# Optimization experiments

Hardware: AMD Instinct MI355X
Metric: run time of the kernel (lower is better)

## Reference

```python
import jax, jax.numpy as jnp
import numpy as np

D_STATE = 16
DT_RANK = 48
D_CONV = 4
EPS = 1e-5


def rmsnorm(x, w):
    return x * jax.lax.rsqrt(jnp.mean(x * x, axis=-1, keepdims=True) + EPS) * w


def causal_dw_conv(u, w, b):
    # u: [B,T,D], w: [D,K] depthwise causal kernel, b: [D]
    B, T, D = u.shape
    K = w.shape[1]
    up = jnp.pad(u, ((0, 0), (K - 1, 0), (0, 0)))
    acc = jnp.zeros_like(u)
    for k in range(K):  # K=4, tiny fixed loop
        acc = acc + up[:, k:k + T, :] * w[:, k]
    return acc + b


def mamba_mixer(h, ipw, cw, cb, xpw, dpw, dpb, alog, dpar, opw):
    # h: [B,T,d_model]
    B, T, _ = h.shape
    xz = h @ ipw.T                       # [B,T,2*d_inner]
    u, z = jnp.split(xz, 2, axis=-1)     # each [B,T,d_inner]
    u = jax.nn.silu(causal_dw_conv(u, cw, cb))
    xp = u @ xpw.T                       # [B,T,dt_rank+2*d_state]
    dt = xp[..., :DT_RANK]
    Bm = xp[..., DT_RANK:DT_RANK + D_STATE]
    Cm = xp[..., DT_RANK + D_STATE:]
    delta = jax.nn.softplus(dt @ dpw.T + dpb)      # [B,T,d_inner]
    A = -jnp.exp(alog)                              # [d_inner, d_state], negative
    dA = jnp.exp(delta[..., None] * A)              # [B,T,d_inner,d_state] in (0,1)
    dBu = (delta * u)[..., None] * Bm[:, :, None, :]
    # time-major for scan
    dA_t = jnp.moveaxis(dA, 1, 0)
    dBu_t = jnp.moveaxis(dBu, 1, 0)
    C_t = jnp.moveaxis(Cm, 1, 0)

    def step(hst, inp):
        a, bu, c = inp
        hst = a * hst + bu                          # [B,d_inner,d_state]
        y = jnp.einsum('bdn,bn->bd', hst, c)
        return hst, y

    h0 = jnp.zeros((B, u.shape[-1], D_STATE), u.dtype)
    _, ys = jax.lax.scan(step, h0, (dA_t, dBu_t, C_t))
    y = jnp.moveaxis(ys, 0, 1) + u * dpar           # skip via D
    y = y * jax.nn.silu(z)                          # gate
    return y @ opw.T                                # [B,T,d_model]


def setup_inputs() -> dict:
    key = jax.random.key(0)
    ks = jax.random.split(key, 16)
    L, d_model, d_inner = 4, 768, 1536
    B, C, T = 4, 256, 512
    s = 0.02
    return {
        'x': jax.random.normal(ks[0], (B, C, T), jnp.float32),
        'in_proj_w': jax.random.normal(ks[1], (L, 2 * d_inner, d_model), jnp.float32) * s,
        'conv_w': jax.random.normal(ks[2], (L, d_inner, D_CONV), jnp.float32) * 0.3,
        'conv_b': jnp.zeros((L, d_inner), jnp.float32),
        'x_proj_w': jax.random.normal(ks[3], (L, DT_RANK + 2 * D_STATE, d_inner), jnp.float32) * s,
        'dt_proj_w': jax.random.normal(ks[4], (L, d_inner, DT_RANK), jnp.float32) * 0.1,
        'dt_proj_b': jax.random.normal(ks[5], (L, d_inner), jnp.float32) * 0.1 - 4.0,
        'A_log': jax.random.uniform(ks[6], (L, d_inner, D_STATE), jnp.float32, 0.0, 1.5),
        'D_param': jax.random.uniform(ks[7], (L, d_inner), jnp.float32),
        'out_proj_w': jax.random.normal(ks[8], (L, d_model, d_inner), jnp.float32) * s,
        'norm_w': jnp.ones((L, d_model), jnp.float32),
        'norm_f_w': jnp.ones((d_model,), jnp.float32),
        'inp_w': jax.random.normal(ks[9], (d_model, C), jnp.float32) * s,
        'inp_b': jnp.zeros((d_model,), jnp.float32),
        'cls_w': jax.random.normal(ks[10], (10, d_model), jnp.float32) * s,
        'cls_b': jnp.zeros((10,), jnp.float32),
    }


def reference(x, in_proj_w, conv_w, conv_b, x_proj_w, dt_proj_w, dt_proj_b,
              A_log, D_param, out_proj_w, norm_w, norm_f_w,
              inp_w, inp_b, cls_w, cls_b):
    # x: (B, C, T) -> (B, T, C)
    xt = jnp.transpose(x, (0, 2, 1))
    h = xt @ inp_w.T + inp_b                # [B,T,d_model]
    hidden = h
    residual = None
    L = in_proj_w.shape[0]
    for l in range(L):
        residual = hidden if residual is None else hidden + residual
        normed = rmsnorm(residual, norm_w[l])
        hidden = mamba_mixer(normed, in_proj_w[l], conv_w[l], conv_b[l],
                             x_proj_w[l], dt_proj_w[l], dt_proj_b[l],
                             A_log[l], D_param[l], out_proj_w[l])
    residual = hidden + residual
    hidden = rmsnorm(residual, norm_f_w)
    pooled = hidden.mean(axis=1)            # [B,d_model]
    logits = pooled @ cls_w.T + cls_b       # [B,num_labels]
    return logits
```

## Files before the change

### kernel.cpp

```cpp
#include <hip/hip_runtime.h>
#include <math.h>

#define D_MODEL 768
#define D_INNER 1536
#define B_SZ 4
#define T_SZ 512
#define ROWS (B_SZ*T_SZ)
#define XP_N 80
#define CH 32
#define CT 16
#define XS 8
#define XKC (D_INNER/XS)
#define OS 4
#define OKC (D_INNER/OS)
#define MN_OUT (ROWS*768)

typedef __attribute__((ext_vector_type(8))) short bf16x8;
typedef __attribute__((ext_vector_type(4))) float f32x4;

#define GLL(g, l) __builtin_amdgcn_global_load_lds( \
    (const __attribute__((address_space(1))) void*)(g), \
    (__attribute__((address_space(3))) void*)(l), 16, 0, 0)

__device__ __forceinline__ float sigmoidf_(float x){ return 1.0f/(1.0f+__expf(-x)); }
__device__ __forceinline__ float siluf_(float x){ return x*sigmoidf_(x); }
__device__ __forceinline__ unsigned short f2bf(float f){
  unsigned u = __builtin_bit_cast(unsigned, f);
  u = (u + 0x7FFFu + ((u >> 16) & 1u)) >> 16;
  return (unsigned short)u;
}

__global__ __launch_bounds__(256) void gemm_bf16(
    const unsigned short* __restrict__ A, const unsigned short* __restrict__ Wb,
    float* __restrict__ C, int M, int N, int K)
{
  __shared__ unsigned short As[64*32];
  __shared__ unsigned short Ws[128*32];
  const int tid = threadIdx.x;
  const int bm = blockIdx.y*64, bn = blockIdx.x*128;
  const int wave = tid >> 6, lane = tid & 63;
  const int wn = wave*32;
  const int fr = lane & 15, quad = lane >> 4;
  f32x4 acc[4][2] = {};
  const int chunk = wave*64 + lane;
  const int row0 = chunk >> 2;
  const int khp  = chunk & 3;
  const int khl  = (khp + 4 - ((row0 >> 1) & 3)) & 3;
  const unsigned short* Ag = A  + (size_t)(bm + row0)*K + khl*8;
  const unsigned short* Wg = Wb + (size_t)(bn + row0)*K + khl*8;
  const size_t rstep = (size_t)64*K;
  unsigned short* ldsA = As + wave*512;
  unsigned short* ldsW = Ws + wave*512;

  for (int k0 = 0; k0 < K; k0 += 32){
    GLL(Ag + k0,          ldsA);
    GLL(Wg + k0,          ldsW);
    GLL(Wg + rstep + k0,  ldsW + 2048);
    __syncthreads();
    bf16x8 a[4], b[2];
    #pragma unroll
    for (int i=0;i<4;i++){
      const int row = i*16 + fr;
      a[i] = *(const bf16x8*)(As + row*32 + (((quad + (row>>1)) & 3)*8));
    }
    #pragma unroll
    for (int j=0;j<2;j++){
      const int row = wn + j*16 + fr;
      b[j] = *(const bf16x8*)(Ws + row*32 + (((quad + (row>>1)) & 3)*8));
    }
    #pragma unroll
    for (int i=0;i<4;i++)
      #pragma unroll
      for (int j=0;j<2;j++)
        acc[i][j] = __builtin_amdgcn_mfma_f32_16x16x32_bf16(a[i], b[j], acc[i][j], 0, 0, 0);
    __syncthreads();
  }
  #pragma unroll
  for (int i=0;i<4;i++){
    #pragma unroll
    for (int r=0;r<4;r++){
      const int row = bm + i*16 + quad*4 + r;
      float* Cp = C + (size_t)row*N + bn + wn + fr;
      #pragma unroll
      for (int j=0;j<2;j++)
        Cp[j*16] = acc[i][j][r];
    }
  }
}

__global__ __launch_bounds__(256) void gemm_bf16_sk(
    const unsigned short* __restrict__ A, const unsigned short* __restrict__ Wb,
    float* __restrict__ P0, float* __restrict__ P1, int M, int N, int K)
{
  __shared__ unsigned short As[64*32];
  __shared__ unsigned short Ws[128*32];
  const int tid = threadIdx.x;
  const int bm = blockIdx.y*64, bn = blockIdx.x*128;
  const int s = blockIdx.z;
  const int koff = s*OKC;
  const int wave = tid >> 6, lane = tid & 63;
  const int wn = wave*32;
  const int fr = lane & 15, quad = lane >> 4;
  f32x4 acc[4][2] = {};
  const int chunk = wave*64 + lane;
  const int row0 = chunk >> 2;
  const int khp  = chunk & 3;
  const int khl  = (khp + 4 - ((row0 >> 1) & 3)) & 3;
  const unsigned short* Ag = A  + (size_t)(bm + row0)*K + koff + khl*8;
  const unsigned short* Wg = Wb + (size_t)(bn + row0)*K + koff + khl*8;
  const size_t rstep = (size_t)64*K;
  unsigned short* ldsA = As + wave*512;
  unsigned short* ldsW = Ws + wave*512;

  for (int k0 = 0; k0 < OKC; k0 += 32){
    GLL(Ag + k0,          ldsA);
    GLL(Wg + k0,          ldsW);
    GLL(Wg + rstep + k0,  ldsW + 2048);
    __syncthreads();
    bf16x8 a[4], b[2];
    #pragma unroll
    for (int i=0;i<4;i++){
      const int row = i*16 + fr;
      a[i] = *(const bf16x8*)(As + row*32 + (((quad + (row>>1)) & 3)*8));
    }
    #pragma unroll
    for (int j=0;j<2;j++){
      const int row = wn + j*16 + fr;
      b[j] = *(const bf16x8*)(Ws + row*32 + (((quad + (row>>1)) & 3)*8));
    }
    #pragma unroll
    for (int i=0;i<4;i++)
      #pragma unroll
      for (int j=0;j<2;j++)
        acc[i][j] = __builtin_amdgcn_mfma_f32_16x16x32_bf16(a[i], b[j], acc[i][j], 0, 0, 0);
    __syncthreads();
  }
  float* Cb = (s < 2 ? P0 : P1) + (size_t)(s & 1)*MN_OUT;
  #pragma unroll
  for (int i=0;i<4;i++){
    #pragma unroll
    for (int r=0;r<4;r++){
      const int row = bm + i*16 + quad*4 + r;
      float* Cp = Cb + (size_t)row*N + bn + wn + fr;
      #pragma unroll
      for (int j=0;j<2;j++)
        Cp[j*16] = acc[i][j][r];
    }
  }
}

__global__ __launch_bounds__(256) void sgemm_input(
    const float* __restrict__ x, const float* __restrict__ W,
    const float* __restrict__ bias, float* __restrict__ C)
{
  __shared__ float As[16][64];
  __shared__ float Wsh[16][64];
  const int bm = blockIdx.y*64, bn = blockIdx.x*64;
  const int b = bm >> 9, t0 = bm & (T_SZ-1);
  const int tid = threadIdx.x;
  const int tx = tid & 15, ty = tid >> 4;
  const int lm = tid & 63, lk = (tid >> 6) << 2;
  float acc[4][4] = {};
  const float* Wp = W + (size_t)(bn+lm)*256 + lk;
  const float* xb = x + ((size_t)b*256)*512 + t0 + lm;
  for (int k0 = 0; k0 < 256; k0 += 16){
    #pragma unroll
    for (int i=0;i<4;i++)
      As[lk+i][lm] = xb[(size_t)(k0+lk+i)*512];
    float4 wv = *(const float4*)(Wp + k0);
    Wsh[lk+0][lm]=wv.x; Wsh[lk+1][lm]=wv.y; Wsh[lk+2][lm]=wv.z; Wsh[lk+3][lm]=wv.w;
    __syncthreads();
    #pragma unroll
    for (int k = 0; k < 16; k++){
      float a[4], w[4];
      #pragma unroll
      for (int i=0;i<4;i++) a[i] = As[k][ty*4+i];
      #pragma unroll
      for (int j=0;j<4;j++) w[j] = Wsh[k][tx*4+j];
      #pragma unroll
      for (int i=0;i<4;i++)
        #pragma unroll
        for (int j=0;j<4;j++)
          acc[i][j] += a[i]*w[j];
    }
    __syncthreads();
  }
  #pragma unroll
  for (int i=0;i<4;i++){
    const int r = bm + ty*4 + i;
    #pragma unroll
    for (int j=0;j<4;j++){
      const int n = bn + tx*4 + j;
      C[(size_t)r*768 + n] = acc[i][j] + bias[n];
    }
  }
}

__global__ __launch_bounds__(256) void xproj_conv_splitk(
    const float* __restrict__ xz, const float* __restrict__ cw,
    const float* __restrict__ cb, const float* __restrict__ W,
    float* __restrict__ part)
{
  __shared__ float As[16][64];
  __shared__ float Wsh[16][80];
  const int bm = blockIdx.x*64;
  const int s = blockIdx.y;
  const int koff = s*XKC;
  const int tid = threadIdx.x;
  const int tx = tid & 15, ty = tid >> 4;
  const int lm = tid & 63, lk = (tid >> 6) << 2;
  float acc[4][5] = {};
  const int row = bm + lm;
  const int t = row & (T_SZ-1);
  for (int k0 = 0; k0 < XKC; k0 += 16){
    const int d0 = koff + k0 + lk;
    float4 cbv = *(const float4*)(cb + d0);
    float cba[4] = {cbv.x, cbv.y, cbv.z, cbv.w};
    float4 tp3 = *(const float4*)(xz + (size_t)row*3072 + d0);
    float4 tp0 = (t>=3) ? *(const float4*)(xz + (size_t)(row-3)*3072 + d0) : make_float4(0.f,0.f,0.f,0.f);
    float4 tp1 = (t>=2) ? *(const float4*)(xz + (size_t)(row-2)*3072 + d0) : make_float4(0.f,0.f,0.f,0.f);
    float4 tp2 = (t>=1) ? *(const float4*)(xz + (size_t)(row-1)*3072 + d0) : make_float4(0.f,0.f,0.f,0.f);
    float a0[4]={tp0.x,tp0.y,tp0.z,tp0.w}, a1[4]={tp1.x,tp1.y,tp1.z,tp1.w};
    float a2[4]={tp2.x,tp2.y,tp2.z,tp2.w}, a3[4]={tp3.x,tp3.y,tp3.z,tp3.w};
    #pragma unroll
    for (int i=0;i<4;i++){
      const float4 w4 = *(const float4*)(cw + (size_t)(d0+i)*4);
      float a = cba[i];
      a += a0[i]*w4.x; a += a1[i]*w4.y; a += a2[i]*w4.z; a += a3[i]*w4.w;
      As[lk+i][lm] = siluf_(a);
    }
    for (int i = tid; i < 320; i += 256){
      const int wr = i % 80, wk = (i / 80) << 2;
      float4 wv = *(const float4*)(W + (size_t)wr*D_INNER + koff + k0 + wk);
      Wsh[wk+0][wr]=wv.x; Wsh[wk+1][wr]=wv.y; Wsh[wk+2][wr]=wv.z; Wsh[wk+3][wr]=wv.w;
    }
    __syncthreads();
    #pragma unroll
    for (int k = 0; k < 16; k++){
      float a[4], w[5];
      #pragma unroll
      for (int i=0;i<4;i++) a[i] = As[k][ty*4+i];
      #pragma unroll
      for (int j=0;j<5;j++) w[j] = Wsh[k][tx*5+j];
      #pragma unroll
      for (int i=0;i<4;i++)
        #pragma unroll
        for (int j=0;j<5;j++)
          acc[i][j] += a[i]*w[j];
    }
    __syncthreads();
  }
  #pragma unroll
  for (int i=0;i<4;i++){
    const int r = bm + ty*4 + i;
    #pragma unroll
    for (int j=0;j<5;j++){
      const int n = tx*5 + j;
      part[((size_t)s*ROWS + r)*XP_N + n] = acc[i][j];
    }
  }
}

__global__ __launch_bounds__(256) void dtproj_fused(
    const float* __restrict__ part, const float* __restrict__ W,
    const float* __restrict__ bias, float* __restrict__ delta,
    float* __restrict__ xpbc)
// ... 46 lines not shown
  #pragma unroll
  for (int i=0;i<4;i++){
    const int r = bm + ty*4 + i;
    #pragma unroll
    for (int j=0;j<4;j++){
      const int n = bn + tx*4 + j;
      float v = acc[i][j] + bias[n];
      v = (v > 20.f) ? v : log1pf(__expf(v));
      delta[(size_t)r*D_INNER + n] = v;
    }
  }
}

__global__ __launch_bounds__(256) void scan_pass1(
    const float* __restrict__ delta, const float* __restrict__ xz,
    const float* __restrict__ xpbc, const float* __restrict__ alog,
    const float* __restrict__ cw, const float* __restrict__ cb,
    float* __restrict__ Pend, float* __restrict__ Hend)
{
  const int d = blockIdx.x*256 + threadIdx.x;
  const int b = blockIdx.y, c = blockIdx.z;
  float4 t0 = *(const float4*)(alog + d*16 + 0);
  float4 t1 = *(const float4*)(alog + d*16 + 4);
  float4 t2 = *(const float4*)(alog + d*16 + 8);
  float4 t3 = *(const float4*)(alog + d*16 + 12);
  float Av[16] = {t0.x,t0.y,t0.z,t0.w,t1.x,t1.y,t1.z,t1.w,
                  t2.x,t2.y,t2.z,t2.w,t3.x,t3.y,t3.z,t3.w};
  float h[16];
  #pragma unroll
  for (int n=0;n<16;n++){ Av[n] = -__expf(Av[n]); h[n]=0.f; }
  float sdv = 0.f;
  const size_t row0 = (size_t)b*T_SZ + (size_t)c*CT;
  const float* dp  = delta + row0*D_INNER + d;
  const float* xp0 = xz    + row0*3072 + d;
  const float* bp  = xpbc  + row0*32;
  const float4 cwv = *(const float4*)(cw + (size_t)d*4);
  const float cbv = cb[d];
  float xm3, xm2, xm1;
  if (c == 0){ xm3 = xm2 = xm1 = 0.f; }
  else { xm3 = xp0[-3*3072]; xm2 = xp0[-2*3072]; xm1 = xp0[-1*3072]; }
  #pragma unroll 4
  for (int tt=0; tt<CT; tt++){
    const float dv = dp[(size_t)tt*D_INNER];
    const float xc = xp0[(size_t)tt*3072];
    float ua = cbv;
    ua += xm3*cwv.x; ua += xm2*cwv.y; ua += xm1*cwv.z; ua += xc*cwv.w;
    const float uv = siluf_(ua);
    xm3 = xm2; xm2 = xm1; xm1 = xc;
    const float4 B0 = *(const float4*)(bp + (size_t)tt*32);
    const float4 B1 = *(const float4*)(bp + (size_t)tt*32 + 4);
    const float4 B2 = *(const float4*)(bp + (size_t)tt*32 + 8);
    const float4 B3 = *(const float4*)(bp + (size_t)tt*32 + 12);
    const float Bv[16] = {B0.x,B0.y,B0.z,B0.w,B1.x,B1.y,B1.z,B1.w,
                          B2.x,B2.y,B2.z,B2.w,B3.x,B3.y,B3.z,B3.w};
    const float du = dv*uv;
    sdv += dv;
    #pragma unroll
    for (int n=0;n<16;n++){
      const float dA = __expf(dv*Av[n]);
      h[n] = dA*h[n] + du*Bv[n];
    }
  }
  float P[16];
  #pragma unroll
  for (int n=0;n<16;n++) P[n] = __expf(Av[n]*sdv);
  float* Pp = Pend + ((size_t)(b*CH+c)*D_INNER + d)*16;
  float* Hp = Hend + ((size_t)(b*CH+c)*D_INNER + d)*16;
  *(float4*)(Pp+ 0) = make_float4(P[0],P[1],P[2],P[3]);
  *(float4*)(Pp+ 4) = make_float4(P[4],P[5],P[6],P[7]);
  *(float4*)(Pp+ 8) = make_float4(P[8],P[9],P[10],P[11]);
  *(float4*)(Pp+12) = make_float4(P[12],P[13],P[14],P[15]);
  *(float4*)(Hp+ 0) = make_float4(h[0],h[1],h[2],h[3]);
  *(float4*)(Hp+ 4) = make_float4(h[4],h[5],h[6],h[7]);
  *(float4*)(Hp+ 8) = make_float4(h[8],h[9],h[10],h[11]);
  *(float4*)(Hp+12) = make_float4(h[12],h[13],h[14],h[15]);
}

__global__ __launch_bounds__(256) void scan_combine(
    const float* __restrict__ Pend, const float* __restrict__ Hend,
    float* __restrict__ Hin)
{
  const int gid = blockIdx.x*256 + threadIdx.x;
  const int b = gid / (D_INNER*16);
  const int r = gid % (D_INNER*16);
  const size_t base = (size_t)b*CH*D_INNER*16 + r;
  const size_t step = (size_t)D_INNER*16;
  float h = 0.f;
  Hin[base] = 0.f;
  #pragma unroll
  for (int c=0; c<CH-1; c++){
    h = Pend[base + (size_t)c*step]*h + Hend[base + (size_t)c*step];
    Hin[base + (size_t)(c+1)*step] = h;
  }
}

__global__ __launch_bounds__(256) void scan_pass3(
    const float* __restrict__ delta, const float* __restrict__ xz,
    const float* __restrict__ xpbc, const float* __restrict__ alog,
    const float* __restrict__ cw, const float* __restrict__ cb,
    const float* __restrict__ Dp, const float* __restrict__ Hin,
    unsigned short* __restrict__ yb)
{
  const int d = blockIdx.x*256 + threadIdx.x;
  const int b = blockIdx.y, c = blockIdx.z;
  float4 t0 = *(const float4*)(alog + d*16 + 0);
  float4 t1 = *(const float4*)(alog + d*16 + 4);
  float4 t2 = *(const float4*)(alog + d*16 + 8);
  float4 t3 = *(const float4*)(alog + d*16 + 12);
  float Av[16] = {t0.x,t0.y,t0.z,t0.w,t1.x,t1.y,t1.z,t1.w,
                  t2.x,t2.y,t2.z,t2.w,t3.x,t3.y,t3.z,t3.w};
  #pragma unroll
  for (int n=0;n<16;n++) Av[n] = -__expf(Av[n]);
  const float* Hp = Hin + ((size_t)(b*CH+c)*D_INNER + d)*16;
  float4 h0 = *(const float4*)(Hp+0);
  float4 h1 = *(const float4*)(Hp+4);
  float4 h2 = *(const float4*)(Hp+8);
  float4 h3 = *(const float4*)(Hp+12);
  float h[16] = {h0.x,h0.y,h0.z,h0.w,h1.x,h1.y,h1.z,h1.w,
                 h2.x,h2.y,h2.z,h2.w,h3.x,h3.y,h3.z,h3.w};
  const float Dv = Dp[d];
  const size_t row0 = (size_t)b*T_SZ + (size_t)c*CT;
  const float* dp  = delta + row0*D_INNER + d;
  const float* xp0 = xz    + row0*3072 + d;
  const float* zp  = xz    + row0*3072 + 1536 + d;
  const float* bp  = xpbc  + row0*32;
  unsigned short* yp = yb + row0*D_INNER + d;
  const float4 cwv = *(const float4*)(cw + (size_t)d*4);
  const float cbv = cb[d];
  float xm3, xm2, xm1;
  if (c == 0){ xm3 = xm2 = xm1 = 0.f; }
  else { xm3 = xp0[-3*3072]; xm2 = xp0[-2*3072]; xm1 = xp0[-1*3072]; }
  #pragma unroll 2
  for (int tt=0; tt<CT; tt++){
    const float dv = dp[(size_t)tt*D_INNER];
    const float xc = xp0[(size_t)tt*3072];
    const float zv = zp[(size_t)tt*3072];
    float ua = cbv;
    ua += xm3*cwv.x; ua += xm2*cwv.y; ua += xm1*cwv.z; ua += xc*cwv.w;
    const float uv = siluf_(ua);
    xm3 = xm2; xm2 = xm1; xm1 = xc;
    const float4 B0 = *(const float4*)(bp + (size_t)tt*32);
    const float4 B1 = *(const float4*)(bp + (size_t)tt*32 + 4);
    const float4 B2 = *(const float4*)(bp + (size_t)tt*32 + 8);
    const float4 B3 = *(const float4*)(bp + (size_t)tt*32 + 12);
    const float4 C0 = *(const float4*)(bp + (size_t)tt*32 + 16);
    const float4 C1 = *(const float4*)(bp + (size_t)tt*32 + 20);
    const float4 C2 = *(const float4*)(bp + (size_t)tt*32 + 24);
    const float4 C3 = *(const float4*)(bp + (size_t)tt*32 + 28);
    const float Bv[16] = {B0.x,B0.y,B0.z,B0.w,B1.x,B1.y,B1.z,B1.w,
                          B2.x,B2.y,B2.z,B2.w,B3.x,B3.y,B3.z,B3.w};
    const float Cv[16] = {C0.x,C0.y,C0.z,C0.w,C1.x,C1.y,C1.z,C1.w,
                          C2.x,C2.y,C2.z,C2.w,C3.x,C3.y,C3.z,C3.w};
    const float du = dv*uv;
    float p = 0.f;
    #pragma unroll
    for (int n=0;n<16;n++){
      const float dA = __expf(dv*Av[n]);
      h[n] = dA*h[n] + du*Bv[n];
      p += h[n]*Cv[n];
    }
    yp[(size_t)tt*D_INNER] = f2bf((p + uv*Dv)*siluf_(zv));
  }
}

__global__ __launch_bounds__(256) void fused_norm_cast(
    float* __restrict__ resid, const float* __restrict__ P0, const float* __restrict__ P1,
    const float* __restrict__ w, unsigned short* __restrict__ obf, float* __restrict__ ofp,
    const float* __restrict__ cin1, unsigned short* __restrict__ co1, int cn1, int cnb1,
    const float* __restrict__ cin2, unsigned short* __restrict__ co2, int cn2)
{
  const int blk = blockIdx.x;
  if (blk >= 2048){
    const int cb = blk - 2048;
    const float* in; unsigned short* o; int i4;
    if (cb < cnb1){ in = cin1; o = co1; i4 = (cb*256 + threadIdx.x)*4; if (i4 >= cn1) return; }
    else { in = cin2; o = co2; i4 = ((cb-cnb1)*256 + threadIdx.x)*4; if (i4 >= cn2) return; }
    float4 v = *(const float4*)(in + i4);
    ushort4 r;
    r.x = f2bf(v.x); r.y = f2bf(v.y); r.z = f2bf(v.z); r.w = f2bf(v.w);
    *(ushort4*)(o + i4) = r;
    return;
  }
  const int row = blk;
  const int tid = threadIdx.x;
  float v[3];
  float ss = 0.f;
  #pragma unroll
  for (int i=0;i<3;i++){
    const int c = tid + i*256;
    const size_t idx = (size_t)row*768 + c;
    float r = resid[idx];
    if (P0) r += (P0[idx] + P0[MN_OUT + idx]) + (P1[idx] + P1[MN_OUT + idx]);
    v[i] = r;
    ss += r*r;
  }
  #pragma unroll
  for (int off=32; off>=1; off>>=1) ss += __shfl_xor(ss, off);
  __shared__ float sred[4];
  const int lane = tid & 63, wv = tid >> 6;
  if (lane == 0) sred[wv] = ss;
  __syncthreads();
  const float tot = sred[0]+sred[1]+sred[2]+sred[3];
  const float scale = rsqrtf(tot*(1.0f/768.0f) + 1e-5f);
  #pragma unroll
  for (int i=0;i<3;i++){
    const int c = tid + i*256;
    const size_t idx = (size_t)row*768 + c;
    if (P0) resid[idx] = v[i];
    const float o = v[i]*scale*w[c];
    if (obf) obf[idx] = f2bf(o);
    else     ofp[idx] = o;
  }
}

__global__ __launch_bounds__(256) void pool_partial(const float* __restrict__ normed,
                                                    float* __restrict__ part){
  const int i = blockIdx.x*256 + threadIdx.x;
  const int s = blockIdx.y;
  const int b = i / 768, m = i % 768;
  float sum = 0.f;
  const float* p = normed + ((size_t)b*T_SZ + s*32)*768 + m;
  #pragma unroll
  for (int t=0; t<32; t++) sum += p[(size_t)t*768];
  part[s*3072 + i] = sum;
}

__global__ __launch_bounds__(256) void pool_cls(const float* __restrict__ part,
                                                const float* __restrict__ cw,
                                                const float* __restrict__ cb,
                                                float* __restrict__ out){
  __shared__ float ls[768];
  const int b = blockIdx.x;
  const int tid = threadIdx.x;
  #pragma unroll
  for (int i=0;i<3;i++){
    const int m = tid + i*256;
    float s = 0.f;
    #pragma unroll
    for (int c=0;c<16;c++) s += part[c*3072 + b*768 + m];
    ls[m] = s * (1.0f/T_SZ);
  }
  __syncthreads();
  const int wave = tid >> 6, lane = tid & 63;
  for (int o = wave; o < 10; o += 4){
    float s = 0.f;
    for (int k = lane; k < 768; k += 64) s += ls[k]*cw[o*768 + k];
    #pragma unroll
    for (int off=32; off>=1; off>>=1) s += __shfl_xor(s, off);
    if (lane == 0) out[b*10 + o] = s + cb[o];
  }
}

extern "C" void kernel_launch(void* const* d_in, const int* in_sizes, int n_in,
                              void* d_out, int out_size, void* d_ws, size_t ws_size,
                              hipStream_t stream) {
  const float* x         = (const float*)d_in[0];
  const float* in_proj_w = (const float*)d_in[1];
  const float* conv_w    = (const float*)d_in[2];
  const float* conv_b    = (const float*)d_in[3];
  const float* x_proj_w  = (const float*)d_in[4];
  const float* dt_proj_w = (const float*)d_in[5];
  const float* dt_proj_b = (const float*)d_in[6];
  const float* A_log     = (const float*)d_in[7];
  const float* D_param   = (const float*)d_in[8];
  const float* out_proj_w= (const float*)d_in[9];
  const float* norm_w    = (const float*)d_in[10];
  const float* norm_f_w  = (const float*)d_in[11];
  const float* inp_w     = (const float*)d_in[12];
  const float* inp_b     = (const float*)d_in[13];
  const float* cls_w     = (const float*)d_in[14];
  const float* cls_b     = (const float*)d_in[15];
  float* out = (float*)d_out;

  char* ws = (char*)d_ws;
  auto carve = [&](size_t nelem)->float* {
    float* p = (float*)ws;
    ws += ((nelem*sizeof(float) + 255)/256)*256;
    return p;
  };
  float* resid  = carve((size_t)ROWS*768);
  float* normed = carve((size_t)ROWS*768);
  float* xz     = carve((size_t)ROWS*3072);
  float* ucv    = carve((size_t)ROWS*1536);
  float* xpbc   = carve((size_t)ROWS*32);
  float* delta  = carve((size_t)ROWS*1536);
  float* ybf_f  = carve((size_t)ROWS*1536/2);
  float* wbi_f  = carve((size_t)(3072*768)/2);
  float* wbo_f  = carve((size_t)(768*1536)/2);
  float* Pend   = carve((size_t)B_SZ*CH*D_INNER*16);
  float* Hend   = carve((size_t)B_SZ*CH*D_INNER*16);
  float* Hin    = carve((size_t)B_SZ*CH*D_INNER*16);
  float* xpart  = carve((size_t)XS*ROWS*XP_N);
  float* ppool  = carve((size_t)16*3072);

  unsigned short* normedb = (unsigned short*)normed;
  unsigned short* ybf = (unsigned short*)ybf_f;
  unsigned short* wbi = (unsigned short*)wbi_f;
  unsigned short* wbo = (unsigned short*)wbo_f;

  sgemm_input<<<dim3(12,32), 256, 0, stream>>>(x, inp_w, inp_b, resid);

  for (int l = 0; l < 4; l++){
    fused_norm_cast<<<2048 + 2304 + 1152, 256, 0, stream>>>(
        resid, l ? delta : nullptr, l ? ucv : nullptr,
        norm_w + (size_t)l*768, normedb, nullptr,
        in_proj_w + (size_t)l*3072*768, wbi, 3072*768, 2304,
        out_proj_w + (size_t)l*768*1536, wbo, 768*1536);
    gemm_bf16<<<dim3(24,32), 256, 0, stream>>>(normedb, wbi, xz, ROWS, 3072, 768);
    xproj_conv_splitk<<<dim3(32,XS), 256, 0, stream>>>(
        xz, conv_w + (size_t)l*1536*4, conv_b + (size_t)l*1536,
        x_proj_w + (size_t)l*XP_N*1536, xpart);
    dtproj_fused<<<dim3(32,32), 256, 0, stream>>>(
        xpart, dt_proj_w + (size_t)l*1536*48, dt_proj_b + (size_t)l*1536, delta, xpbc);
    scan_pass1<<<dim3(6,B_SZ,CH-1), 256, 0, stream>>>(
        delta, xz, xpbc, A_log + (size_t)l*1536*16,
        conv_w + (size_t)l*1536*4, conv_b + (size_t)l*1536, Pend, Hend);
    scan_combine<<<(B_SZ*D_INNER*16)/256, 256, 0, stream>>>(Pend, Hend, Hin);
    scan_pass3<<<dim3(6,B_SZ,CH), 256, 0, stream>>>(
        delta, xz, xpbc, A_log + (size_t)l*1536*16,
        conv_w + (size_t)l*1536*4, conv_b + (size_t)l*1536,
        D_param + (size_t)l*1536, Hin, ybf);
    gemm_bf16_sk<<<dim3(6,32,OS), 256, 0, stream>>>(ybf, wbo, delta, ucv, ROWS, 768, 1536);
  }

  fused_norm_cast<<<2048, 256, 0, stream>>>(
      resid, delta, ucv, norm_f_w, nullptr, normed,
      nullptr, nullptr, 0, 0, nullptr, nullptr, 0);
  pool_partial<<<dim3(12,16), 256, 0, stream>>>(normed, ppool);
  pool_cls<<<4, 256, 0, stream>>>(ppool, cls_w, cls_b, out);
}
```

Measured before the change: 818.5 us.

## Fuse whole forward pass into one cooperative persistent megakernel with grid syncs

```diff
diff --git a/kernel.cpp b/kernel.cpp
--- a/kernel.cpp
+++ b/kernel.cpp
@@ -1,5 +1,8 @@
 #include <hip/hip_runtime.h>
+#include <hip/hip_cooperative_groups.h>
 #include <math.h>
+
+namespace cg = cooperative_groups;
 
 #define D_MODEL 768
 #define D_INNER 1536
@@ -14,6 +17,7 @@
 #define OS 4
 #define OKC (D_INNER/OS)
 #define MN_OUT (ROWS*768)
+#define GRID 512
 
 typedef __attribute__((ext_vector_type(8))) short bf16x8;
 typedef __attribute__((ext_vector_type(4))) float f32x4;
@@ -28,6 +32,563 @@
   unsigned u = __builtin_bit_cast(unsigned, f);
   u = (u + 0x7FFFu + ((u >> 16) & 1u)) >> 16;
   return (unsigned short)u;
+}
+
+struct MP {
+  const float *x, *in_proj_w, *conv_w, *conv_b, *x_proj_w, *dt_proj_w, *dt_proj_b,
+              *A_log, *D_param, *out_proj_w, *norm_w, *norm_f_w, *inp_w, *inp_b,
+              *cls_w, *cls_b;
+  float *out;
+  float *resid, *normed, *xz, *ucv, *xpbc, *delta, *Pend, *Hend, *Hin, *xpart, *ppool;
+  unsigned short *ybf, *wbi, *wbo;
+};
+
+__global__ __launch_bounds__(256, 2) void mega(MP p)
+{
+  cg::grid_group gg = cg::this_grid();
+  __shared__ __align__(16) char smem[12544];
+  const int bid = threadIdx.y*0 + blockIdx.x;
+  const int G = gridDim.x;
+  const int tid = threadIdx.x;
+  unsigned short* normedb = (unsigned short*)p.normed;
+
+  for (int task = bid; task < 384 + 9216 + 4608; task += G){
+    if (task < 384){
+      float (*As)[64]  = (float(*)[64])smem;
+      float (*Wsh)[64] = (float(*)[64])(smem + 4096);
+      const int bn = (task % 12)*64, bm = (task / 12)*64;
+      const int b = bm >> 9, t0 = bm & (T_SZ-1);
+      const int tx = tid & 15, ty = tid >> 4;
+      const int lm = tid & 63, lk = (tid >> 6) << 2;
+      float acc[4][4] = {};
+      const float* Wp = p.inp_w + (size_t)(bn+lm)*256 + lk;
+      const float* xb = p.x + ((size_t)b*256)*512 + t0 + lm;
+      for (int k0 = 0; k0 < 256; k0 += 16){
+        #pragma unroll
+        for (int i=0;i<4;i++)
+          As[lk+i][lm] = xb[(size_t)(k0+lk+i)*512];
+        float4 wv = *(const float4*)(Wp + k0);
+        Wsh[lk+0][lm]=wv.x; Wsh[lk+1][lm]=wv.y; Wsh[lk+2][lm]=wv.z; Wsh[lk+3][lm]=wv.w;
+        __syncthreads();
+        #pragma unroll
+        for (int k = 0; k < 16; k++){
+          float a[4], w[4];
+          #pragma unroll
+          for (int i=0;i<4;i++) a[i] = As[k][ty*4+i];
+          #pragma unroll
+          for (int j=0;j<4;j++) w[j] = Wsh[k][tx*4+j];
+          #pragma unroll
+          for (int i=0;i<4;i++)
+            #pragma unroll
+            for (int j=0;j<4;j++)
+              acc[i][j] += a[i]*w[j];
+        }
+        __syncthreads();
+      }
+      #pragma unroll
+      for (int i=0;i<4;i++){
+        const int r = bm + ty*4 + i;
+        #pragma unroll
+        for (int j=0;j<4;j++){
+          const int n = bn + tx*4 + j;
+          p.resid[(size_t)r*768 + n] = acc[i][j] + p.inp_b[n];
+        }
+      }
+    } else if (task < 384 + 9216){
+      const int t2 = task - 384;
+      const int l = t2 / 2304;
+      const int i4 = ((t2 % 2304)*256 + tid)*4;
+      float4 v = *(const float4*)(p.in_proj_w + (size_t)l*2359296 + i4);
+      ushort4 r;
+      r.x = f2bf(v.x); r.y = f2bf(v.y); r.z = f2bf(v.z); r.w = f2bf(v.w);
+      *(ushort4*)(p.wbi + (size_t)l*2359296 + i4) = r;
+    } else {
+      const int t3 = task - 384 - 9216;
+      const int l = t3 / 1152;
+      const int i4 = ((t3 % 1152)*256 + tid)*4;
+      float4 v = *(const float4*)(p.out_proj_w + (size_t)l*1179648 + i4);
+      ushort4 r;
+      r.x = f2bf(v.x); r.y = f2bf(v.y); r.z = f2bf(v.z); r.w = f2bf(v.w);
+      *(ushort4*)(p.wbo + (size_t)l*1179648 + i4) = r;
+    }
+  }
+  gg.sync();
+
+  for (int l = 0; l < 4; ++l){
+    const unsigned short* wbi = p.wbi + (size_t)l*2359296;
+    const unsigned short* wbo = p.wbo + (size_t)l*1179648;
+    const float* cw   = p.conv_w   + (size_t)l*6144;
+    const float* cb   = p.conv_b   + (size_t)l*1536;
+    const float* alog = p.A_log    + (size_t)l*24576;
+    const float* nw   = p.norm_w   + (size_t)l*768;
+
+    for (int task = bid; task < 2048; task += G){
+      const int row = task;
+      float v[3]; float ss = 0.f;
+      #pragma unroll
+      for (int i=0;i<3;i++){
+        const int c = tid + i*256;
+        const size_t idx = (size_t)row*768 + c;
+        float r = p.resid[idx];
+        if (l) r += (p.delta[idx] + p.delta[MN_OUT + idx]) + (p.ucv[idx] + p.ucv[MN_OUT + idx]);
+        v[i] = r; ss += r*r;
+      }
+      #pragma unroll
+      for (int off=32; off>=1; off>>=1) ss += __shfl_xor(ss, off);
+      float* sred = (float*)smem;
+      const int lane = tid & 63, wv = tid >> 6;
+      if (lane == 0) sred[wv] = ss;
+      __syncthreads();
+      const float tot = sred[0]+sred[1]+sred[2]+sred[3];
+      const float scale = rsqrtf(tot*(1.0f/768.0f) + 1e-5f);
+      __syncthreads();
+      #pragma unroll
+      for (int i=0;i<3;i++){
+        const int c = tid + i*256;
+        const size_t idx = (size_t)row*768 + c;
+        if (l) p.resid[idx] = v[i];
+        normedb[idx] = f2bf(v[i]*scale*nw[c]);
+      }
+    }
+    gg.sync();
+
+    for (int task = bid; task < 768; task += G){
+      unsigned short* As = (unsigned short*)smem;
+      unsigned short* Ws = (unsigned short*)(smem + 4096);
+      const int bn = (task % 24)*128, bm = (task / 24)*64;
+      const int wave = tid >> 6, lane = tid & 63;
+      const int wn = wave*32;
+      const int fr = lane & 15, quad = lane >> 4;
+      f32x4 acc[4][2] = {};
+      const int chunk = wave*64 + lane;
+      const int row0 = chunk >> 2;
+      const int khp  = chunk & 3;
+      const int khl  = (khp + 4 - ((row0 >> 1) & 3)) & 3;
+      const unsigned short* Ag = normedb + (size_t)(bm + row0)*768 + khl*8;
+      const unsigned short* Wg = wbi     + (size_t)(bn + row0)*768 + khl*8;
+      const size_t rstep = (size_t)64*768;
+      unsigned short* ldsA = As + wave*512;
+      unsigned short* ldsW = Ws + wave*512;
+      for (int k0 = 0; k0 < 768; k0 += 32){
+        GLL(Ag + k0,          ldsA);
+        GLL(Wg + k0,          ldsW);
+        GLL(Wg + rstep + k0,  ldsW + 2048);
+        __syncthreads();
+        bf16x8 a[4], b2[2];
+        #pragma unroll
+        for (int i=0;i<4;i++){
+          const int row = i*16 + fr;
+          a[i] = *(const bf16x8*)(As + row*32 + (((quad + (row>>1)) & 3)*8));
+        }
+        #pragma unroll
+        for (int j=0;j<2;j++){
+          const int row = wn + j*16 + fr;
+          b2[j] = *(const bf16x8*)(Ws + row*32 + (((quad + (row>>1)) & 3)*8));
+        }
+        #pragma unroll
+        for (int i=0;i<4;i++)
+          #pragma unroll
+          for (int j=0;j<2;j++)
+            acc[i][j] = __builtin_amdgcn_mfma_f32_16x16x32_bf16(a[i], b2[j], acc[i][j], 0, 0, 0);
+        __syncthreads();
+      }
+      #pragma unroll
+      for (int i=0;i<4;i++){
+        #pragma unroll
+        for (int r=0;r<4;r++){
+          const int row = bm + i*16 + quad*4 + r;
+          float* Cp = p.xz + (size_t)row*3072 + bn + wn + fr;
+          #pragma unroll
+          for (int j=0;j<2;j++)
+            Cp[j*16] = acc[i][j][r];
+        }
+      }
+    }
+    gg.sync();
+
+    for (int task = bid; task < 256; task += G){
+      float (*As)[64]  = (float(*)[64])smem;
+      float (*Wsh)[80] = (float(*)[80])(smem + 4096);
+      const int bm = (task % 32)*64;
+      const int s = task / 32;
+      const int koff = s*XKC;
+      const int tx = tid & 15, ty = tid >> 4;
+      const int lm = tid & 63, lk = (tid >> 6) << 2;
+      float acc[4][5] = {};
+      const int row = bm + lm;
+      const int t = row & (T_SZ-1);
+      const float* Wx = p.x_proj_w + (size_t)l*122880;
+      for (int k0 = 0; k0 < XKC; k0 += 16){
+        const int d0 = koff + k0 + lk;
+        float4 cbv = *(const float4*)(cb + d0);
+        float cba[4] = {cbv.x, cbv.y, cbv.z, cbv.w};
+        float4 tp3 = *(const float4*)(p.xz + (size_t)row*3072 + d0);
+        float4 tp0 = (t>=3) ? *(const float4*)(p.xz + (size_t)(row-3)*3072 + d0) : make_float4(0.f,0.f,0.f,0.f);
+        float4 tp1 = (t>=2) ? *(const float4*)(p.xz + (size_t)(row-2)*3072 + d0) : make_float4(0.f,0.f,0.f,0.f);
+        float4 tp2 = (t>=1) ? *(const float4*)(p.xz + (size_t)(row-1)*3072 + d0) : make_float4(0.f,0.f,0.f,0.f);
+        float a0[4]={tp0.x,tp0.y,tp0.z,tp0.w}, a1[4]={tp1.x,tp1.y,tp1.z,tp1.w};
+        float a2[4]={tp2.x,tp2.y,tp2.z,tp2.w}, a3[4]={tp3.x,tp3.y,tp3.z,tp3.w};
+        #pragma unroll
+        for (int i=0;i<4;i++){
+          const float4 w4 = *(const float4*)(cw + (size_t)(d0+i)*4);
+          float a = cba[i];
+          a += a0[i]*w4.x; a += a1[i]*w4.y; a += a2[i]*w4.z; a += a3[i]*w4.w;
+          As[lk+i][lm] = siluf_(a);
+        }
+        for (int i = tid; i < 320; i += 256){
+          const int wr = i % 80, wk = (i / 80) << 2;
+          float4 wv = *(const float4*)(Wx + (size_t)wr*D_INNER + koff + k0 + wk);
+          Wsh[wk+0][wr]=wv.x; Wsh[wk+1][wr]=wv.y; Wsh[wk+2][wr]=wv.z; Wsh[wk+3][wr]=wv.w;
+        }
+        __syncthreads();
+        #pragma unroll
+        for (int k = 0; k < 16; k++){
+          float a[4], w[5];
+          #pragma unroll
+          for (int i=0;i<4;i++) a[i] = As[k][ty*4+i];
+          #pragma unroll
+          for (int j=0;j<5;j++) w[j] = Wsh[k][tx*5+j];
+          #pragma unroll
+          for (int i=0;i<4;i++)
+            #pragma unroll
+            for (int j=0;j<5;j++)
+              acc[i][j] += a[i]*w[j];
+        }
+        __syncthreads();
+      }
+      #pragma unroll
+      for (int i=0;i<4;i++){
+        const int r = bm + ty*4 + i;
+        #pragma unroll
+        for (int j=0;j<5;j++){
+          const int n = tx*5 + j;
+          p.xpart[((size_t)s*ROWS + r)*XP_N + n] = acc[i][j];
+        }
+      }
+    }
+    gg.sync();
+
+    for (int task = bid; task < 1024; task += G){
+      if (task >= 768){
+        const int i = (task - 768)*256 + tid;
+        const int r = i >> 5, cc = i & 31;
+        float ssum = 0.f;
+        #pragma unroll
+        for (int s2=0;s2<XS;s2++)
+          ssum += p.xpart[((size_t)s2*ROWS + r)*XP_N + 48 + cc];
+        p.xpbc[(size_t)r*32 + cc] = ssum;
+        continue;
+      }
+      float (*As)[64]  = (float(*)[64])smem;
+      float (*Wsh)[64] = (float(*)[64])(smem + 4096);
+      const int bn = (task % 24)*64, bm = (task / 24)*64;
+      const int tx = tid & 15, ty = tid >> 4;
+      const int lm = tid & 63, lk = (tid >> 6) << 2;
+      float acc[4][4] = {};
+      const float* Ap = p.xpart + (size_t)(bm+lm)*XP_N + lk;
+      const float* Wp = p.dt_proj_w + (size_t)l*73728 + (size_t)(bn+lm)*48 + lk;
+      for (int k0 = 0; k0 < 48; k0 += 16){
+        float4 av = make_float4(0.f,0.f,0.f,0.f);
+        #pragma unroll
+        for (int s2=0;s2<XS;s2++){
+          const float4 pv = *(const float4*)(Ap + (size_t)s2*ROWS*XP_N + k0);
+          av.x += pv.x; av.y += pv.y; av.z += pv.z; av.w += pv.w;
+        }
+        float4 wv = *(const float4*)(Wp + k0);
+        As[lk+0][lm]=av.x; As[lk+1][lm]=av.y; As[lk+2][lm]=av.z; As[lk+3][lm]=av.w;
+        Wsh[lk+0][lm]=wv.x; Wsh[lk+1][lm]=wv.y; Wsh[lk+2][lm]=wv.z; Wsh[lk+3][lm]=wv.w;
+        __syncthreads();
+        #pragma unroll
+        for (int k = 0; k < 16; k++){
+          float a[4], w[4];
+          #pragma unroll
+          for (int i=0;i<4;i++) a[i] = As[k][ty*4+i];
+          #pragma unroll
+          for (int j=0;j<4;j++) w[j] = Wsh[k][tx*4+j];
+          #pragma unroll
+          for (int i=0;i<4;i++)
+            #pragma unroll
+            for (int j=0;j<4;j++)
+              acc[i][j] += a[i]*w[j];
+        }
+        __syncthreads();
+      }
+      const float* bias = p.dt_proj_b + (size_t)l*1536;
+      #pragma unroll
+      for (int i=0;i<4;i++){
+        const int r = bm + ty*4 + i;
+        #pragma unroll
+        for (int j=0;j<4;j++){
+          const int n = bn + tx*4 + j;
+          float v = acc[i][j] + bias[n];
+          v = (v > 20.f) ? v : log1pf(__expf(v));
+          p.delta[(size_t)r*D_INNER + n] = v;
+        }
+      }
+    }
+    gg.sync();
+
+    for (int task = bid; task < 744; task += G){
+      const int d = (task % 6)*256 + tid;
+      const int b = (task / 6) % 4, c = task / 24;
+      float4 t0 = *(const float4*)(alog + d*16 + 0);
+      float4 t1 = *(const float4*)(alog + d*16 + 4);
+      float4 t2 = *(const float4*)(alog + d*16 + 8);
+      float4 t3 = *(const float4*)(alog + d*16 + 12);
+      float Av[16] = {t0.x,t0.y,t0.z,t0.w,t1.x,t1.y,t1.z,t1.w,
+                      t2.x,t2.y,t2.z,t2.w,t3.x,t3.y,t3.z,t3.w};
+      float h[16];
+      #pragma unroll
+      for (int n=0;n<16;n++){ Av[n] = -__expf(Av[n]); h[n]=0.f; }
+      float sdv = 0.f;
+      const size_t row0 = (size_t)b*T_SZ + (size_t)c*CT;
+      const float* dp  = p.delta + row0*D_INNER + d;
+      const float* xp0 = p.xz    + row0*3072 + d;
+      const float* bp  = p.xpbc  + row0*32;
+      const float4 cwv = *(const float4*)(cw + (size_t)d*4);
+      const float cbv = cb[d];
+      float xm3, xm2, xm1;
+      if (c == 0){ xm3 = xm2 = xm1 = 0.f; }
+      else { xm3 = xp0[-3*3072]; xm2 = xp0[-2*3072]; xm1 = xp0[-1*3072]; }
+      #pragma unroll 4
+      for (int tt=0; tt<CT; tt++){
+        const float dv = dp[(size_t)tt*D_INNER];
+        const float xc = xp0[(size_t)tt*3072];
+        float ua = cbv;
+        ua += xm3*cwv.x; ua += xm2*cwv.y; ua += xm1*cwv.z; ua += xc*cwv.w;
+        const float uv = siluf_(ua);
+        xm3 = xm2; xm2 = xm1; xm1 = xc;
+        const float4 B0 = *(const float4*)(bp + (size_t)tt*32);
+        const float4 B1 = *(const float4*)(bp + (size_t)tt*32 + 4);
+        const float4 B2 = *(const float4*)(bp + (size_t)tt*32 + 8);
+        const float4 B3 = *(const float4*)(bp + (size_t)tt*32 + 12);
+        const float Bv[16] = {B0.x,B0.y,B0.z,B0.w,B1.x,B1.y,B1.z,B1.w,
+                              B2.x,B2.y,B2.z,B2.w,B3.x,B3.y,B3.z,B3.w};
+        const float du = dv*uv;
+        sdv += dv;
+        #pragma unroll
+        for (int n=0;n<16;n++){
+          const float dA = __expf(dv*Av[n]);
+          h[n] = dA*h[n] + du*Bv[n];
+        }
+      }
+      float P[16];
+      #pragma unroll
+      for (int n=0;n<16;n++) P[n] = __expf(Av[n]*sdv);
+      float* Pp = p.Pend + ((size_t)(b*CH+c)*D_INNER + d)*16;
+      float* Hp = p.Hend + ((size_t)(b*CH+c)*D_INNER + d)*16;
+      *(float4*)(Pp+ 0) = make_float4(P[0],P[1],P[2],P[3]);
+      *(float4*)(Pp+ 4) = make_float4(P[4],P[5],P[6],P[7]);
+      *(float4*)(Pp+ 8) = make_float4(P[8],P[9],P[10],P[11]);
+      *(float4*)(Pp+12) = make_float4(P[12],P[13],P[14],P[15]);
+      *(float4*)(Hp+ 0) = make_float4(h[0],h[1],h[2],h[3]);
+      *(float4*)(Hp+ 4) = make_float4(h[4],h[5],h[6],h[7]);
+      *(float4*)(Hp+ 8) = make_float4(h[8],h[9],h[10],h[11]);
+      *(float4*)(Hp+12) = make_float4(h[12],h[13],h[14],h[15]);
+    }
+    gg.sync();
+
+    for (int task = bid; task < 384; task += G){
+      const int gid = task*256 + tid;
+      const int b = gid / (D_INNER*16);
+      const int r = gid % (D_INNER*16);
+      const size_t base = (size_t)b*CH*D_INNER*16 + r;
+      const size_t step = (size_t)D_INNER*16;
+      float h = 0.f;
+      p.Hin[base] = 0.f;
+      #pragma unroll
+      for (int c=0; c<CH-1; c++){
+        h = p.Pend[base + (size_t)c*step]*h + p.Hend[base + (size_t)c*step];
+        p.Hin[base + (size_t)(c+1)*step] = h;
+      }
+    }
+    gg.sync();
+
+    for (int task = bid; task < 768; task += G){
+      const int d = (task % 6)*256 + tid;
+      const int b = (task / 6) % 4, c = task / 24;
+      float4 t0 = *(const float4*)(alog + d*16 + 0);
+      float4 t1 = *(const float4*)(alog + d*16 + 4);
+      float4 t2 = *(const float4*)(alog + d*16 + 8);
+      float4 t3 = *(const float4*)(alog + d*16 + 12);
+      float Av[16] = {t0.x,t0.y,t0.z,t0.w,t1.x,t1.y,t1.z,t1.w,
+                      t2.x,t2.y,t2.z,t2.w,t3.x,t3.y,t3.z,t3.w};
+      #pragma unroll
+      for (int n=0;n<16;n++) Av[n] = -__expf(Av[n]);
+      const float* Hp = p.Hin + ((size_t)(b*CH+c)*D_INNER + d)*16;
+      float4 h0 = *(const float4*)(Hp+0);
+      float4 h1 = *(const float4*)(Hp+4);
+      float4 h2 = *(const float4*)(Hp+8);
+      float4 h3 = *(const float4*)(Hp+12);
+      float h[16] = {h0.x,h0.y,h0.z,h0.w,h1.x,h1.y,h1.z,h1.w,
+                     h2.x,h2.y,h2.z,h2.w,h3.x,h3.y,h3.z,h3.w};
+      const float Dv = p.D_param[(size_t)l*1536 + d];
+      const size_t row0 = (size_t)b*T_SZ + (size_t)c*CT;
+      const float* dp  = p.delta + row0*D_INNER + d;
+      const float* xp0 = p.xz    + row0*3072 + d;
+      const float* zp  = p.xz    + row0*3072 + 1536 + d;
+      const float* bp  = p.xpbc  + row0*32;
+      unsigned short* yp = p.ybf + row0*D_INNER + d;
+      const float4 cwv = *(const float4*)(cw + (size_t)d*4);
+      const float cbv = cb[d];
+      float xm3, xm2, xm1;
+      if (c == 0){ xm3 = xm2 = xm1 = 0.f; }
+      else { xm3 = xp0[-3*3072]; xm2 = xp0[-2*3072]; xm1 = xp0[-1*3072]; }
+      #pragma unroll 2
+      for (int tt=0; tt<CT; tt++){
+        const float dv = dp[(size_t)tt*D_INNER];
+        const float xc = xp0[(size_t)tt*3072];
+        const float zv = zp[(size_t)tt*3072];
+        float ua = cbv;
+        ua += xm3*cwv.x; ua += xm2*cwv.y; ua += xm1*cwv.z; ua += xc*cwv.w;
+        const float uv = siluf_(ua);
+        xm3 = xm2; xm2 = xm1; xm1 = xc;
+        const float4 B0 = *(const float4*)(bp + (size_t)tt*32);
+        const float4 B1 = *(const float4*)(bp + (size_t)tt*32 + 4);
+        const float4 B2 = *(const float4*)(bp + (size_t)tt*32 + 8);
+        const float4 B3 = *(const float4*)(bp + (size_t)tt*32 + 12);
+        const float4 C0 = *(const float4*)(bp + (size_t)tt*32 + 16);
+        const float4 C1 = *(const float4*)(bp + (size_t)tt*32 + 20);
+        const float4 C2 = *(const float4*)(bp + (size_t)tt*32 + 24);
+        const float4 C3 = *(const float4*)(bp + (size_t)tt*32 + 28);
+        const float Bv[16] = {B0.x,B0.y,B0.z,B0.w,B1.x,B1.y,B1.z,B1.w,
+                              B2.x,B2.y,B2.z,B2.w,B3.x,B3.y,B3.z,B3.w};
+        const float Cv[16] = {C0.x,C0.y,C0.z,C0.w,C1.x,C1.y,C1.z,C1.w,
+                              C2.x,C2.y,C2.z,C2.w,C3.x,C3.y,C3.z,C3.w};
+        const float du = dv*uv;
+        float pp = 0.f;
+        #pragma unroll
+        for (int n=0;n<16;n++){
+          const float dA = __expf(dv*Av[n]);
+          h[n] = dA*h[n] + du*Bv[n];
+          pp += h[n]*Cv[n];
+        }
+        yp[(size_t)tt*D_INNER] = f2bf((pp + uv*Dv)*siluf_(zv));
+      }
+    }
+    gg.sync();
+
+    for (int task = bid; task < 768; task += G){
+      unsigned short* As = (unsigned short*)smem;
+      unsigned short* Ws = (unsigned short*)(smem + 4096);
+      const int s = task / 192;
+      const int rr = task % 192;
+      const int bn = (rr % 6)*128, bm = (rr / 6)*64;
+      const int koff = s*OKC;
+      const int wave = tid >> 6, lane = tid & 63;
+      const int wn = wave*32;
+      const int fr = lane & 15, quad = lane >> 4;
+      f32x4 acc[4][2] = {};
+      const int chunk = wave*64 + lane;
+      const int row0 = chunk >> 2;
+      const int khp  = chunk & 3;
+      const int khl  = (khp + 4 - ((row0 >> 1) & 3)) & 3;
+      const unsigned short* Ag = p.ybf + (size_t)(bm + row0)*1536 + koff + khl*8;
+      const unsigned short* Wg = wbo   + (size_t)(bn + row0)*1536 + koff + khl*8;
+      const size_t rstep = (size_t)64*1536;
+      unsigned short* ldsA = As + wave*512;
+      unsigned short* ldsW = Ws + wave*512;
+      for (int k0 = 0; k0 < OKC; k0 += 32){
+        GLL(Ag + k0,          ldsA);
+        GLL(Wg + k0,          ldsW);
+        GLL(Wg + rstep + k0,  ldsW + 2048);
+        __syncthreads();
+        bf16x8 a[4], b2[2];
+        #pragma unroll
+        for (int i=0;i<4;i++){
+          const int row = i*16 + fr;
+          a[i] = *(const bf16x8*)(As + row*32 + (((quad + (row>>1)) & 3)*8));
+        }
+        #pragma unroll
+        for (int j=0;j<2;j++){
+          const int row = wn + j*16 + fr;
+          b2[j] = *(const bf16x8*)(Ws + row*32 + (((quad + (row>>1)) & 3)*8));
+        }
+        #pragma unroll
+        for (int i=0;i<4;i++)
+          #pragma unroll
+          for (int j=0;j<2;j++)
+            acc[i][j] = __builtin_amdgcn_mfma_f32_16x16x32_bf16(a[i], b2[j], acc[i][j], 0, 0, 0);
+        __syncthreads();
+      }
+      float* Cb = (s < 2 ? p.delta : p.ucv) + (size_t)(s & 1)*MN_OUT;
+      #pragma unroll
+      for (int i=0;i<4;i++){
+        #pragma unroll
+        for (int r=0;r<4;r++){
+          const int row = bm + i*16 + quad*4 + r;
+          float* Cp = Cb + (size_t)row*768 + bn + wn + fr;
+          #pragma unroll
+          for (int j=0;j<2;j++)
+            Cp[j*16] = acc[i][j][r];
+        }
+      }
+    }
+    gg.sync();
+  }
+
+  for (int task = bid; task < 2048; task += G){
+    const int row = task;
+    float v[3]; float ss = 0.f;
+    #pragma unroll
+    for (int i=0;i<3;i++){
+      const int c = tid + i*256;
+      const size_t idx = (size_t)row*768 + c;
+      float r = p.resid[idx];
+      r += (p.delta[idx] + p.delta[MN_OUT + idx]) + (p.ucv[idx] + p.ucv[MN_OUT + idx]);
+      v[i] = r; ss += r*r;
+    }
+    #pragma unroll
+    for (int off=32; off>=1; off>>=1) ss += __shfl_xor(ss, off);
+    float* sred = (float*)smem;
+    const int lane = tid & 63, wv = tid >> 6;
+    if (lane == 0) sred[wv] = ss;
+    __syncthreads();
+    const float tot = sred[0]+sred[1]+sred[2]+sred[3];
+    const float scale = rsqrtf(tot*(1.0f/768.0f) + 1e-5f);
+    __syncthreads();
+    #pragma unroll
+    for (int i=0;i<3;i++){
+      const int c = tid + i*256;
+      const size_t idx = (size_t)row*768 + c;
+      p.normed[idx] = v[i]*scale*p.norm_f_w[c];
+    }
+  }
+  gg.sync();
+
+  for (int task = bid; task < 192; task += G){
+    const int i = (task % 12)*256 + tid;
+    const int s = task / 12;
+    const int b = i / 768, m = i % 768;
+    float sum = 0.f;
+    const float* pp = p.normed + ((size_t)b*T_SZ + s*32)*768 + m;
+    #pragma unroll
+    for (int t=0; t<32; t++) sum += pp[(size_t)t*768];
+    p.ppool[s*3072 + i] = sum;
+  }
+  gg.sync();
+
+  for (int task = bid; task < 4; task += G){
+    float* ls = (float*)smem;
+    const int b = task;
+    #pragma unroll
+    for (int i=0;i<3;i++){
+      const int m = tid + i*256;
+      float s = 0.f;
+      #pragma unroll
+      for (int c=0;c<16;c++) s += p.ppool[c*3072 + b*768 + m];
+      ls[m] = s * (1.0f/T_SZ);
+    }
+    __syncthreads();
+    const int wave = tid >> 6, lane = tid & 63;
+    for (int o = wave; o < 10; o += 4){
+      float s = 0.f;
+      for (int k = lane; k < 768; k += 64) s += ls[k]*p.cls_w[o*768 + k];
+      #pragma unroll
+      for (int off=32; off>=1; off>>=1) s += __shfl_xor(s, off);
+      if (lane == 0) p.out[b*10 + o] = s + p.cls_b[o];
+    }
+  }
 }
 
 __global__ __launch_bounds__(256) void gemm_bf16(
@@ -51,7 +612,6 @@
   const size_t rstep = (size_t)64*K;
   unsigned short* ldsA = As + wave*512;
   unsigned short* ldsW = Ws + wave*512;
-
   for (int k0 = 0; k0 < K; k0 += 32){
     GLL(Ag + k0,          ldsA);
     GLL(Wg + k0,          ldsW);
@@ -111,7 +671,6 @@
   const size_t rstep = (size_t)64*K;
   unsigned short* ldsA = As + wave*512;
   unsigned short* ldsW = Ws + wave*512;
-
   for (int k0 = 0; k0 < OKC; k0 += 32){
     GLL(Ag + k0,          ldsA);
     GLL(Wg + k0,          ldsW);
@@ -464,14 +1023,14 @@
     const float Cv[16] = {C0.x,C0.y,C0.z,C0.w,C1.x,C1.y,C1.z,C1.w,
                           C2.x,C2.y,C2.z,C2.w,C3.x,C3.y,C3.z,C3.w};
     const float du = dv*uv;
-    float p = 0.f;
+    float pp = 0.f;
     #pragma unroll
     for (int n=0;n<16;n++){
       const float dA = __expf(dv*Av[n]);
       h[n] = dA*h[n] + du*Bv[n];
-      p += h[n]*Cv[n];
-    }
-    yp[(size_t)tt*D_INNER] = f2bf((p + uv*Dv)*siluf_(zv));
+      pp += h[n]*Cv[n];
+    }
+    yp[(size_t)tt*D_INNER] = f2bf((pp + uv*Dv)*siluf_(zv));
   }
 }
 
@@ -566,78 +1125,81 @@
 extern "C" void kernel_launch(void* const* d_in, const int* in_sizes, int n_in,
                               void* d_out, int out_size, void* d_ws, size_t ws_size,
                               hipStream_t stream) {
-  const float* x         = (const float*)d_in[0];
-  const float* in_proj_w = (const float*)d_in[1];
-  const float* conv_w    = (const float*)d_in[2];
-  const float* conv_b    = (const float*)d_in[3];
-  const float* x_proj_w  = (const float*)d_in[4];
-  const float* dt_proj_w = (const float*)d_in[5];
-  const float* dt_proj_b = (const float*)d_in[6];
-  const float* A_log     = (const float*)d_in[7];
-  const float* D_param   = (const float*)d_in[8];
-  const float* out_proj_w= (const float*)d_in[9];
-  const float* norm_w    = (const float*)d_in[10];
-  const float* norm_f_w  = (const float*)d_in[11];
-  const float* inp_w     = (const float*)d_in[12];
-  const float* inp_b     = (const float*)d_in[13];
-  const float* cls_w     = (const float*)d_in[14];
-  const float* cls_b     = (const float*)d_in[15];
-  float* out = (float*)d_out;
-
+  (void)in_sizes; (void)n_in; (void)out_size; (void)ws_size;
   char* ws = (char*)d_ws;
   auto carve = [&](size_t nelem)->float* {
-    float* p = (float*)ws;
+    float* q = (float*)ws;
     ws += ((nelem*sizeof(float) + 255)/256)*256;
-    return p;
+    return q;
   };
-  float* resid  = carve((size_t)ROWS*768);
-  float* normed = carve((size_t)ROWS*768);
-  float* xz     = carve((size_t)ROWS*3072);
-  float* ucv    = carve((size_t)ROWS*1536);
-  float* xpbc   = carve((size_t)ROWS*32);
-  float* delta  = carve((size_t)ROWS*1536);
-  float* ybf_f  = carve((size_t)ROWS*1536/2);
-  float* wbi_f  = carve((size_t)(3072*768)/2);
-  float* wbo_f  = carve((size_t)(768*1536)/2);
-  float* Pend   = carve((size_t)B_SZ*CH*D_INNER*16);
-  float* Hend   = carve((size_t)B_SZ*CH*D_INNER*16);
-  float* Hin    = carve((size_t)B_SZ*CH*D_INNER*16);
-  float* xpart  = carve((size_t)XS*ROWS*XP_N);
-  float* ppool  = carve((size_t)16*3072);
-
-  unsigned short* normedb = (unsigned short*)normed;
-  unsigned short* ybf = (unsigned short*)ybf_f;
-  unsigned short* wbi = (unsigned short*)wbi_f;
-  unsigned short* wbo = (unsigned short*)wbo_f;
-
-  sgemm_input<<<dim3(12,32), 256, 0, stream>>>(x, inp_w, inp_b, resid);
-
+  MP p;
+  p.x         = (const float*)d_in[0];
+  p.in_proj_w = (const float*)d_in[1];
+  p.conv_w    = (const float*)d_in[2];
+  p.conv_b    = (const float*)d_in[3];
+  p.x_proj_w  = (const float*)d_in[4];
+  p.dt_proj_w = (const float*)d_in[5];
+  p.dt_proj_b = (const float*)d_in[6];
+  p.A_log     = (const float*)d_in[7];
+  p.D_param   = (const float*)d_in[8];
+  p.out_proj_w= (const float*)d_in[9];
+  p.norm_w    = (const float*)d_in[10];
+  p.norm_f_w  = (const float*)d_in[11];
+  p.inp_w     = (const float*)d_in[12];
+  p.inp_b     = (const float*)d_in[13];
+  p.cls_w     = (const float*)d_in[14];
+  p.cls_b     = (const float*)d_in[15];
+  p.out       = (float*)d_out;
+
+  p.resid  = carve((size_t)ROWS*768);
+  p.normed = carve((size_t)ROWS*768);
+  p.xz     = carve((size_t)ROWS*3072);
+  p.ucv    = carve((size_t)ROWS*1536);
+  p.xpbc   = carve((size_t)ROWS*32);
+  p.delta  = carve((size_t)ROWS*1536);
+  float* ybf_f = carve((size_t)ROWS*1536/2);
+  float* wbi_f = carve((size_t)4*(3072*768)/2);
+  float* wbo_f = carve((size_t)4*(768*1536)/2);
+  p.Pend   = carve((size_t)B_SZ*CH*D_INNER*16);
+  p.Hend   = carve((size_t)B_SZ*CH*D_INNER*16);
+  p.Hin    = carve((size_t)B_SZ*CH*D_INNER*16);
+  p.xpart  = carve((size_t)XS*ROWS*XP_N);
+  p.ppool  = carve((size_t)16*3072);
+  p.ybf = (unsigned short*)ybf_f;
+  p.wbi = (unsigned short*)wbi_f;
+  p.wbo = (unsigned short*)wbo_f;
+
+  void* args[] = {(void*)&p};
+  hipError_t err = hipLaunchCooperativeKernel(mega, dim3(GRID), dim3(256), args, 0, stream);
+  if (err == hipSuccess) return;
+
+  (void)hipGetLastError();
+  sgemm_input<<<dim3(12,32), 256, 0, stream>>>(p.x, p.inp_w, p.inp_b, p.resid);
   for (int l = 0; l < 4; l++){
     fused_norm_cast<<<2048 + 2304 + 1152, 256, 0, stream>>>(
-        resid, l ? delta : nullptr, l ? ucv : nullptr,
-        norm_w + (size_t)l*768, normedb, nullptr,
-        in_proj_w + (size_t)l*3072*768, wbi, 3072*768, 2304,
-        out_proj_w + (size_t)l*768*1536, wbo, 768*1536);
-    gemm_bf16<<<dim3(24,32), 256, 0, stream>>>(normedb, wbi, xz, ROWS, 3072, 768);
+        p.resid, l ? p.delta : nullptr, l ? p.ucv : nullptr,
+        p.norm_w + (size_t)l*768, (unsigned short*)p.normed, nullptr,
+        p.in_proj_w + (size_t)l*2359296, p.wbi, 2359296, 2304,
+        p.out_proj_w + (size_t)l*1179648, p.wbo, 1179648);
+    gemm_bf16<<<dim3(24,32), 256, 0, stream>>>((unsigned short*)p.normed, p.wbi, p.xz, ROWS, 3072, 768);
     xproj_conv_splitk<<<dim3(32,XS), 256, 0, stream>>>(
-        xz, conv_w + (size_t)l*1536*4, conv_b + (size_t)l*1536,
-        x_proj_w + (size_t)l*XP_N*1536, xpart);
+        p.xz, p.conv_w + (size_t)l*6144, p.conv_b + (size_t)l*1536,
+        p.x_proj_w + (size_t)l*122880, p.xpart);
     dtproj_fused<<<dim3(32,32), 256, 0, stream>>>(
-        xpart, dt_proj_w + (size_t)l*1536*48, dt_proj_b + (size_t)l*1536, delta, xpbc);
+        p.xpart, p.dt_proj_w + (size_t)l*73728, p.dt_proj_b + (size_t)l*1536, p.delta, p.xpbc);
     scan_pass1<<<dim3(6,B_SZ,CH-1), 256, 0, stream>>>(
-        delta, xz, xpbc, A_log + (size_t)l*1536*16,
-        conv_w + (size_t)l*1536*4, conv_b + (size_t)l*1536, Pend, Hend);
-    scan_combine<<<(B_SZ*D_INNER*16)/256, 256, 0, stream>>>(Pend, Hend, Hin);
+        p.delta, p.xz, p.xpbc, p.A_log + (size_t)l*24576,
+        p.conv_w + (size_t)l*6144, p.conv_b + (size_t)l*1536, p.Pend, p.Hend);
+    scan_combine<<<(B_SZ*D_INNER*16)/256, 256, 0, stream>>>(p.Pend, p.Hend, p.Hin);
     scan_pass3<<<dim3(6,B_SZ,CH), 256, 0, stream>>>(
-        delta, xz, xpbc, A_log + (size_t)l*1536*16,
-        conv_w + (size_t)l*1536*4, conv_b + (size_t)l*1536,
-        D_param + (size_t)l*1536, Hin, ybf);
-    gemm_bf16_sk<<<dim3(6,32,OS), 256, 0, stream>>>(ybf, wbo, delta, ucv, ROWS, 768, 1536);
-  }
-
+        p.delta, p.xz, p.xpbc, p.A_log + (size_t)l*24576,
+        p.conv_w + (size_t)l*6144, p.conv_b + (size_t)l*1536,
+        p.D_param + (size_t)l*1536, p.Hin, p.ybf);
+    gemm_bf16_sk<<<dim3(6,32,OS), 256, 0, stream>>>(p.ybf, p.wbo, p.delta, p.ucv, ROWS, 768, 1536);
+  }
   fused_norm_cast<<<2048, 256, 0, stream>>>(
-      resid, delta, ucv, norm_f_w, nullptr, normed,
+      p.resid, p.delta, p.ucv, p.norm_f_w, nullptr, p.normed,
       nullptr, nullptr, 0, 0, nullptr, nullptr, 0);
-  pool_partial<<<dim3(12,16), 256, 0, stream>>>(normed, ppool);
-  pool_cls<<<4, 256, 0, stream>>>(ppool, cls_w, cls_b, out);
-}
+  pool_partial<<<dim3(12,16), 256, 0, stream>>>(p.normed, p.ppool);
+  pool_cls<<<4, 256, 0, stream>>>(p.ppool, p.cls_w, p.cls_b, p.out);
+}
```

Measured after the change: 3.029 ms. +270.0%, slower.
